# Kernel tuning notes

Hardware: AMD Instinct MI355X
Metric: run time of the kernel (lower is better)

Reference implementation:

```python
import jax, jax.numpy as jnp
import numpy as np

K_NEIGHBORS = 32  # n_neighbors, eval mode -> displacement = 0


def setup_inputs() -> dict:
    key = jax.random.key(0)
    ks = jax.random.split(key, 9)
    B, N, F = 1024, 200000, 64
    C, H = 16, 128
    return {
        "x": jax.random.normal(ks[0], (B, F), jnp.float32),
        "X_data": jax.random.normal(ks[1], (N, F), jnp.float32),
        "y": jax.random.uniform(ks[2], (N,), jnp.float32),
        "W_gate": jax.random.normal(ks[3], (F + 1, C), jnp.float32) / np.sqrt(F + 1),
        "b_gate": jax.random.normal(ks[4], (C,), jnp.float32) * 0.01,
        "W1": jax.random.normal(ks[5], (C + F, H), jnp.float32) / np.sqrt(C + F),
        "b1": jax.random.normal(ks[6], (H,), jnp.float32) * 0.01,
        "W_last": jax.random.normal(ks[7], (H, 1), jnp.float32) / np.sqrt(H),
        "b_last": jax.random.normal(ks[8], (1,), jnp.float32) * 0.01,
    }


def reference(x, X_data, y, W_gate, b_gate, W1, b1, W_last, b_last):
    # Euclidean (p=2) cdist via the expanded form: ||a-b||^2 = ||a||^2 + ||b||^2 - 2 a.b
    d2 = (jnp.sum(x * x, axis=1, keepdims=True)
          + jnp.sum(X_data * X_data, axis=1)[None, :]
          - 2.0 * (x @ X_data.T))                      # [B, N]
    dist = jnp.sqrt(jnp.maximum(d2, 0.0))
    # torch.argsort(distances,1)[:, :k] == indices of k smallest distances
    _, idx = jax.lax.top_k(-dist, K_NEIGHBORS)          # [B, K]
    neighbors = X_data[idx]                             # [B, K, F] gather
    neighbors_y = y[idx][..., None]                     # [B, K, 1]
    nf = jnp.concatenate([neighbors, neighbors_y], axis=2)  # [B, K, F+1]
    gated = jnp.tanh(nf @ W_gate + b_gate)              # [B, K, C]
    agg = jnp.sum(gated, axis=1)                        # [B, C]
    o = jnp.concatenate([x, agg], axis=1)               # [B, F+C]
    o = jnp.tanh(o @ W1 + b1)                           # activation_function = tanh
    o = jax.nn.sigmoid(o @ W_last + b_last)             # [B, 1]
    return o
```

## Files before the change

kernel.cpp:

```cpp
#include <hip/hip_runtime.h>
#include <cstdint>

#define FDIM 64
#define KNN 32
#define NBUCKET 256
#define MAXCAP 2048
#define SEG 10
#define OCAP 512

typedef unsigned int u32;
typedef unsigned long long u64;
typedef __attribute__((ext_vector_type(8))) short bf16x8;
typedef __attribute__((ext_vector_type(4))) float f32x4;

__device__ __forceinline__ float load_query(const float* __restrict__ x, int q, float4* xv) {
    const float4* xp = (const float4*)(x + (size_t)q * FDIM);
    float n0 = 0.f, n1 = 0.f, n2 = 0.f, n3 = 0.f;
#pragma unroll
    for (int k = 0; k < 16; ++k) {
        float4 v = xp[k];
        xv[k] = v;
        n0 = fmaf(v.x, v.x, n0); n1 = fmaf(v.y, v.y, n1);
        n2 = fmaf(v.z, v.z, n2); n3 = fmaf(v.w, v.w, n3);
    }
    return (n0 + n1) + (n2 + n3);
}

__device__ __forceinline__ float dot_row(const float4* __restrict__ xv, const float* __restrict__ row) {
    const float4* rv = (const float4*)row;
    float d0 = 0.f, d1 = 0.f, d2 = 0.f, d3 = 0.f;
#pragma unroll
    for (int k = 0; k < 16; ++k) {
        float4 r = rv[k];
        float4 a = xv[k];
        d0 = fmaf(a.x, r.x, d0); d1 = fmaf(a.y, r.y, d1);
        d2 = fmaf(a.z, r.z, d2); d3 = fmaf(a.w, r.w, d3);
    }
    return (d0 + d1) + (d2 + d3);
}

__global__ __launch_bounds__(256) void k_xnorm(const float* __restrict__ X, float* __restrict__ Xn, int N) {
    int i = blockIdx.x * 256 + threadIdx.x;
    if (i >= N) return;
    const float4* r = (const float4*)(X + (size_t)i * FDIM);
    float d0 = 0.f, d1 = 0.f, d2 = 0.f, d3 = 0.f;
#pragma unroll
    for (int k = 0; k < 16; ++k) {
        float4 v = r[k];
        d0 = fmaf(v.x, v.x, d0); d1 = fmaf(v.y, v.y, d1);
        d2 = fmaf(v.z, v.z, d2); d3 = fmaf(v.w, v.w, d3);
    }
    Xn[i] = (d0 + d1) + (d2 + d3);
}

__global__ __launch_bounds__(256) void k_cvtT(const float* __restrict__ src, uint4* __restrict__ dst, int n_u4) {
    int i = blockIdx.x * 256 + threadIdx.x;
    if (i >= n_u4) return;
    int lane = i & 63;
    int kk = (i >> 6) & 1;
    int g = i >> 7;
    int row = g * 16 + (lane & 15);
    int col = kk * 32 + (lane >> 4) * 8;
    const float4* s = (const float4*)(src + (size_t)row * FDIM + col);
    float4 a = s[0], b = s[1];
    ushort o[8];
    const float* f = &a.x;
#pragma unroll
    for (int k = 0; k < 4; ++k) {
        u32 u = __float_as_uint(f[k]);
        o[k] = (ushort)((u + 0x7fffu + ((u >> 16) & 1u)) >> 16);
    }
    const float* gg = &b.x;
#pragma unroll
    for (int k = 0; k < 4; ++k) {
        u32 u = __float_as_uint(gg[k]);
        o[4 + k] = (ushort)((u + 0x7fffu + ((u >> 16) & 1u)) >> 16);
    }
    dst[i] = *(uint4*)o;
}

__global__ __launch_bounds__(256) void k_hist(const float* __restrict__ x, const float* __restrict__ X,
                                              const float* __restrict__ Xn, u32* __restrict__ hist,
                                              int N, int nsamp, int sj) {
    __shared__ unsigned char h8[NBUCKET * 256];
    int t = threadIdx.x;
    u32* h32 = (u32*)h8;
#pragma unroll
    for (int k = 0; k < 64; ++k) h32[k * 256 + t] = 0;
    __syncthreads();
    int q = blockIdx.x * 256 + t;
    float4 xv[16];
    float xn = load_query(x, q, xv);
    for (int j = 0; j < sj; ++j) {
        int s = blockIdx.y * sj + j;
        int p = s * 16;
        if (s < nsamp && p < N) {
            float dp = dot_row(xv, X + (size_t)p * FDIM);
            float d2 = fmaxf(xn + Xn[p] - 2.f * dp, 0.f);
            int b = min(NBUCKET - 1, (int)d2);
            int idx = b * 256 + t;
            unsigned char v = h8[idx];
            h8[idx] = (v == 255u) ? v : (unsigned char)(v + 1);
        }
    }
    __syncthreads();
#pragma unroll
    for (int w = 0; w < 128; ++w) {
        u32 v0 = h8[(2 * w) * 256 + t];
        u32 v1 = h8[(2 * w + 1) * 256 + t];
        if (v0 | v1) atomicAdd(&hist[(size_t)q * 128 + w], v0 | (v1 << 16));
    }
}

__global__ __launch_bounds__(256) void k_thresh(const u32* __restrict__ hist, float* __restrict__ Tq, int B) {
    int q = blockIdx.x * 256 + threadIdx.x;
    if (q >= B) return;
    const u32* h = hist + (size_t)q * 128;
    int cum = 0;
    float T = (float)NBUCKET;
    for (int w = 0; w < 128; ++w) {
        u32 v = h[w];
        cum += (int)(v & 0xffffu);
        if (cum >= KNN) { T = (float)(2 * w + 1); break; }
        cum += (int)(v >> 16);
        if (cum >= KNN) { T = (float)(2 * w + 2); break; }
    }
    Tq[q] = T + 2.0f;
}

__global__ __launch_bounds__(256, 3) void k_sample_d2(
        const uint4* __restrict__ xT, const uint4* __restrict__ XT,
        const float* __restrict__ qn, const float* __restrict__ Xn,
        unsigned char* __restrict__ d2s, int S) {
    int t = threadIdx.x;
    int w = t >> 6, lane = t & 63;
    int G = lane >> 4, r = lane & 15;
    int qg = blockIdx.x;
    int wq = qg * 128 + w * 32;
    int pb = blockIdx.y * 128;

    bf16x8 afr[2][2];
#pragma unroll
    for (int kk = 0; kk < 2; ++kk)
#pragma unroll
        for (int mi = 0; mi < 2; ++mi) {
            uint4 v = xT[(size_t)(((wq >> 4) + mi) * 2 + kk) * 64 + lane];
            afr[kk][mi] = *(bf16x8*)&v;
        }
    float qr[8];
#pragma unroll
    for (int e = 0; e < 8; ++e)
        qr[e] = qn[wq + (e >> 2) * 16 + G * 4 + (e & 3)];

#pragma unroll
    for (int half = 0; half < 2; ++half) {
        int nb = half * 4;
        bf16x8 bfr[4][2];
#pragma unroll
        for (int j = 0; j < 4; ++j) {
            int gp = (pb >> 4) + nb + j;
#pragma unroll
            for (int kk = 0; kk < 2; ++kk) {
                uint4 v = XT[(size_t)(gp * 2 + kk) * 64 + lane];
                bfr[j][kk] = *(bf16x8*)&v;
            }
        }
        float xnv[4];
#pragma unroll
        for (int j = 0; j < 4; ++j) xnv[j] = Xn[pb + (nb + j) * 16 + r];

        f32x4 acc[2][4];
#pragma unroll
        for (int mi = 0; mi < 2; ++mi)
#pragma unroll
            for (int j = 0; j < 4; ++j) acc[mi][j] = (f32x4){0.f, 0.f, 0.f, 0.f};
#pragma unroll
        for (int kk = 0; kk < 2; ++kk)
#pragma unroll
            for (int j = 0; j < 4; ++j) {
                acc[0][j] = __builtin_amdgcn_mfma_f32_16x16x32_bf16(afr[kk][0], bfr[j][kk], acc[0][j], 0, 0, 0);
                acc[1][j] = __builtin_amdgcn_mfma_f32_16x16x32_bf16(afr[kk][1], bfr[j][kk], acc[1][j], 0, 0, 0);
            }
#pragma unroll
        for (int j = 0; j < 4; ++j) {
            int p = pb + (nb + j) * 16 + r;
            float xnp = xnv[j];
#pragma unroll
            for (int e = 0; e < 8; ++e) {
                float d2a = qr[e] + fmaf(-2.f, acc[e >> 2][j][e & 3], xnp);
                int b = (int)d2a;
                b = b < 0 ? 0 : (b > 255 ? 255 : b);
                int q = wq + (e >> 2) * 16 + G * 4 + (e & 3);
                d2s[(size_t)q * S + p] = (unsigned char)b;
            }
        }
    }
}

__global__ __launch_bounds__(256) void k_thresh2(const unsigned char* __restrict__ d2s,
                                                 float* __restrict__ Tq, int S) {
    __shared__ u32 h[NBUCKET];
    int t = threadIdx.x;
    int q = blockIdx.x;
    h[t] = 0;
    __syncthreads();
    const u32* row = (const u32*)(d2s + (size_t)q * S);
    int n4 = S >> 2;
    for (int i = t; i < n4; i += 256) {
        u32 v = row[i];
        atomicAdd(&h[v & 255u], 1u);
        atomicAdd(&h[(v >> 8) & 255u], 1u);
        atomicAdd(&h[(v >> 16) & 255u], 1u);
        atomicAdd(&h[v >> 24], 1u);
    }
    __syncthreads();
    if (t == 0) {
        int cum = 0;
        float T = 256.0f;
        for (int b = 0; b < NBUCKET; ++b) {
            cum += (int)h[b];
            if (cum >= KNN) { T = (float)(b + 1); break; }
        }
        Tq[q] = T + 2.0f;
    }
}

__global__ __launch_bounds__(256, 3) void k_mfma_filter(
        const uint4* __restrict__ xT, const uint4* __restrict__ XT,
        const float* __restrict__ qn, const float* __restrict__ Xn,
        const float* __restrict__ Tf,
        u32* __restrict__ cnt_seg, u32* __restrict__ list_seg,
        u32* __restrict__ ocnt, u32* __restrict__ olist,
        int N, int nStripsPad, int strip) {
    __shared__ u32 ldsCnt[128];

    int t = threadIdx.x;
    int w = t >> 6, lane = t & 63;
    int G = lane >> 4, r = lane & 15;

    int bid = blockIdx.x;
    int qg = (bid >> 3) & 7;
    int sIdx = (bid & 7) | ((bid >> 6) << 3);
    int qbase = qg * 128;
    int wq = qbase + w * 32;

    if (t < 128) ldsCnt[t] = 0;
    __syncthreads();

    bf16x8 afr[2][2];
#pragma unroll
    for (int kk = 0; kk < 2; ++kk)
#pragma unroll
        for (int mi = 0; mi < 2; ++mi) {
            uint4 v = xT[(size_t)(((wq >> 4) + mi) * 2 + kk) * 64 + lane];
            afr[kk][mi] = *(bf16x8*)&v;
        }
    float Tr[8];
#pragma unroll
    for (int e = 0; e < 8; ++e) {
        int rl = wq + (e >> 2) * 16 + G * 4 + (e & 3);
        Tr[e] = Tf[rl] - qn[rl];
    }

    u32* segBase = list_seg + ((size_t)qbase * nStripsPad + (size_t)sIdx) * SEG;

    for (int s = 0; s < strip; ++s) {
        int pb = (sIdx * strip + s) * 128;
        if (pb >= N) break;

#pragma unroll
        for (int half = 0; half < 2; ++half) {
            int nb = half * 4;
            bf16x8 bfr[4][2];
#pragma unroll
            for (int j = 0; j < 4; ++j) {
                int gp = (pb >> 4) + nb + j;
#pragma unroll
                for (int kk = 0; kk < 2; ++kk) {
                    uint4 v = XT[(size_t)(gp * 2 + kk) * 64 + lane];
                    bfr[j][kk] = *(bf16x8*)&v;
                }
            }
            float xnv[4];
#pragma unroll
            for (int j = 0; j < 4; ++j) xnv[j] = Xn[pb + (nb + j) * 16 + r];

            f32x4 acc[2][4];
#pragma unroll
            for (int mi = 0; mi < 2; ++mi)
#pragma unroll
                for (int j = 0; j < 4; ++j) acc[mi][j] = (f32x4){0.f, 0.f, 0.f, 0.f};
#pragma unroll
            for (int kk = 0; kk < 2; ++kk)
#pragma unroll
                for (int j = 0; j < 4; ++j) {
                    acc[0][j] = __builtin_amdgcn_mfma_f32_16x16x32_bf16(afr[kk][0], bfr[j][kk], acc[0][j], 0, 0, 0);
                    acc[1][j] = __builtin_amdgcn_mfma_f32_16x16x32_bf16(afr[kk][1], bfr[j][kk], acc[1][j], 0, 0, 0);
                }
#pragma unroll
            for (int j = 0; j < 4; ++j) {
                int p = pb + (nb + j) * 16 + r;
                float xnp = xnv[j];
                bool c0 = fmaf(-2.f, acc[0][j][0], xnp) < Tr[0];
                bool c1 = fmaf(-2.f, acc[0][j][1], xnp) < Tr[1];
                bool c2 = fmaf(-2.f, acc[0][j][2], xnp) < Tr[2];
                bool c3 = fmaf(-2.f, acc[0][j][3], xnp) < Tr[3];
                bool c4 = fmaf(-2.f, acc[1][j][0], xnp) < Tr[4];
                bool c5 = fmaf(-2.f, acc[1][j][1], xnp) < Tr[5];
                bool c6 = fmaf(-2.f, acc[1][j][2], xnp) < Tr[6];
                bool c7 = fmaf(-2.f, acc[1][j][3], xnp) < Tr[7];
                if ((c0 | c1 | c2 | c3 | c4 | c5 | c6 | c7) && p < N) {
#pragma unroll
                    for (int e = 0; e < 8; ++e) {
                        bool ce = (e == 0) ? c0 : (e == 1) ? c1 : (e == 2) ? c2 : (e == 3) ? c3
                                : (e == 4) ? c4 : (e == 5) ? c5 : (e == 6) ? c6 : c7;
                        if (ce) {
                            int ql = w * 32 + (e >> 2) * 16 + G * 4 + (e & 3);
                            u32 slot = atomicAdd(&ldsCnt[ql], 1u);
                            if (slot < SEG) {
                                segBase[(size_t)ql * nStripsPad * SEG + slot] = (u32)p;
                            } else {
                                u32 gs = atomicAdd(&ocnt[qbase + ql], 1u);
                                if (gs < OCAP) olist[(size_t)(qbase + ql) * OCAP + gs] = (u32)p;
                            }
                        }
                    }
                }
            }
        }
    }

    __syncthreads();
    if (t < 128) cnt_seg[(size_t)(qbase + t) * nStripsPad + sIdx] = min(ldsCnt[t], (u32)SEG);
}

__global__ __launch_bounds__(256) void k_filter_scalar(const float* __restrict__ x, const float* __restrict__ X,
                                                       const float* __restrict__ Xn, const float* __restrict__ Tq,
                                                       u32* __restrict__ cnt, u32* __restrict__ list,
                                                       int N, int cap) {
    int t = threadIdx.x;
    int q = blockIdx.x * 256 + t;
    float4 xv[16];
    float xn = load_query(x, q, xv);
    float T = Tq[q];
    int base = blockIdx.y * 1024;
    int lim = min(1024, N - base);
    for (int j = 0; j < lim; ++j) {
        int p = base + j;
        float dp = dot_row(xv, X + (size_t)p * FDIM);
        float d2 = fmaxf(xn + Xn[p] - 2.f * dp, 0.f);
        if (d2 < T) {
            u32 slot = atomicAdd(&cnt[q], 1u);
            if (slot < (u32)cap) list[(size_t)q * cap + slot] = (u32)p;
        }
    }
}

__global__ __launch_bounds__(256) void k_final(const float* __restrict__ x, const float* __restrict__ X,
                                               const float* __restrict__ y, const float* __restrict__ Xn,
                                               const float* __restrict__ Wg, const float* __restrict__ bg,
                                               const float* __restrict__ W1, const float* __restrict__ b1,
                                               const float* __restrict__ Wl, const float* __restrict__ bl,
                                               const u32* __restrict__ cnt_seg, const u32* __restrict__ list_seg,
                                               const u32* __restrict__ ocnt, const u32* __restrict__ olist,
                                               const u32* __restrict__ cnt_flat, const u32* __restrict__ list_flat,
                                               float* __restrict__ out, int nStripsPad, int cap_flat, int flat,
                                               int N) {
    __shared__ u64 keys[MAXCAP];
    __shared__ u32 nsh;
    __shared__ u64 wk[4];
    __shared__ int wp[4];
    __shared__ u32 sel[KNN];
    __shared__ float gkc[KNN * 16];
    __shared__ float aggc[16];
    __shared__ float red[128];

    int t = threadIdx.x;
    int w = t >> 6, lane = t & 63;
    int q = blockIdx.x;
    int m;

    if (flat) {
        m = (int)min(cnt_flat[q], (u32)cap_flat);
        const u32* lq = list_flat + (size_t)q * cap_flat;
        for (int i = t; i < m; i += 256) keys[i] = lq[i];
    } else {
        if (t == 0) nsh = 0;
        __syncthreads();
        for (int seg = t; seg < nStripsPad; seg += 256) {
            u32 c = cnt_seg[(size_t)q * nStripsPad + seg];
            if (c) {
                u32 base = atomicAdd(&nsh, c);
                const u32* sp = list_seg + ((size_t)q * nStripsPad + seg) * SEG;
                for (u32 j = 0; j < c; ++j) {
                    u32 idx = base + j;
                    if (idx < MAXCAP) keys[idx] = sp[j];
                }
            }
        }
        __syncthreads();
        int m0 = (int)min(nsh, (u32)MAXCAP);
        int oc = (int)min(ocnt[q], (u32)OCAP);
        for (int i = t; i < oc; i += 256)
            if (m0 + i < MAXCAP) keys[m0 + i] = olist[(size_t)q * OCAP + i];
        m = min(m0 + oc, MAXCAP);
    }
    __syncthreads();

    {
        int ch = lane & 15;
        int rsub = lane >> 4;
        float4 xq4 = ((const float4*)(x + (size_t)q * FDIM))[ch];
        float xs = fmaf(xq4.x, xq4.x, fmaf(xq4.y, xq4.y, fmaf(xq4.z, xq4.z, xq4.w * xq4.w)));
        xs += __shfl_xor(xs, 1);
        xs += __shfl_xor(xs, 2);
        xs += __shfl_xor(xs, 4);
        xs += __shfl_xor(xs, 8);
        float xn = xs;
        for (int base = w * 32; base < m; base += 128) {
            int ri[8]; u32 pp[8]; bool val[8]; float4 vv[8];
#pragma unroll
            for (int u = 0; u < 8; ++u) {
                ri[u] = base + u * 4 + rsub;
                val[u] = ri[u] < m;
                pp[u] = val[u] ? (u32)keys[ri[u]] : 0u;
            }
#pragma unroll
            for (int u = 0; u < 8; ++u)
                vv[u] = ((const float4*)(X + (size_t)pp[u] * FDIM))[ch];
#pragma unroll
            for (int u = 0; u < 8; ++u) {
                float part = fmaf(xq4.x, vv[u].x, fmaf(xq4.y, vv[u].y, fmaf(xq4.z, vv[u].z, xq4.w * vv[u].w)));
                part += __shfl_xor(part, 1);
                part += __shfl_xor(part, 2);
                part += __shfl_xor(part, 4);
                part += __shfl_xor(part, 8);
                if (val[u] && ch == 0) {
                    float d2 = fmaxf(xn + Xn[pp[u]] - 2.f * part, 0.f);
                    keys[ri[u]] = ((u64)__float_as_uint(d2) << 32) | pp[u];
                }
            }
        }
    }
    __syncthreads();

    if (m <= 512) {
        if (w == 0) {
            u64 rk[8];
#pragma unroll
            for (int i = 0; i < 8; ++i) {
                int idx = lane + (i << 6);
                rk[i] = (idx < m) ? keys[idx] : ~0ull;
            }
            for (int r = 0; r < KNN; ++r) {
                u64 bk = ~0ull;
                int bs = 0;
#pragma unroll
                for (int i = 0; i < 8; ++i)
                    if (rk[i] < bk) { bk = rk[i]; bs = i; }
                int bo = lane;
#pragma unroll
                for (int off = 1; off < 64; off <<= 1) {
                    u64 ok = __shfl_xor(bk, off);
                    int oo = __shfl_xor(bo, off);
                    if (ok < bk) { bk = ok; bo = oo; }
                }
                if (lane == bo) rk[bs] = ~0ull;
                if (lane == 0) sel[r] = (u32)bk;
            }
        }
        __syncthreads();
    } else {
        for (int r = 0; r < KNN; ++r) {
            u64 bk = ~0ull;
            int bp = -1;
            for (int i = t; i < m; i += 256) {
                u64 k = keys[i];
                if (k < bk) { bk = k; bp = i; }
            }
#pragma unroll
            for (int off = 32; off > 0; off >>= 1) {
                u64 ok = __shfl_down(bk, off);
                int op = __shfl_down(bp, off);
                if (ok < bk) { bk = ok; bp = op; }
            }
            if (lane == 0) { wk[w] = bk; wp[w] = bp; }
            __syncthreads();
            if (t == 0) {
                u64 fb = wk[0];
                int fp = wp[0];
                for (int v = 1; v < 4; ++v)
                    if (wk[v] < fb) { fb = wk[v]; fp = wp[v]; }
                sel[r] = (u32)(fb & 0xffffffffu);
                if (fp >= 0) keys[fp] = ~0ull;
            }
            __syncthreads();
        }
    }

    int c = t & 15, kk = t >> 4;
#pragma unroll
    for (int rep = 0; rep < 2; ++rep) {
        int k = kk + 16 * rep;
        int nb = min((int)sel[k], N - 1);
        const float* Xr = X + (size_t)nb * FDIM;
        float acc = bg[c];
#pragma unroll
        for (int f = 0; f < FDIM; ++f) acc = fmaf(Xr[f], Wg[f * 16 + c], acc);
        acc = fmaf(y[nb], Wg[FDIM * 16 + c], acc);
        gkc[k * 16 + c] = tanhf(acc);
    }
    __syncthreads();
    if (t < 16) {
        float s = 0.f;
#pragma unroll
        for (int k = 0; k < KNN; ++k) s += gkc[k * 16 + t];
        aggc[t] = s;
    }
    __syncthreads();
    if (t < 128) {
        const float* xq = x + (size_t)q * FDIM;
        float acc = b1[t];
#pragma unroll
        for (int f = 0; f < FDIM; ++f) acc = fmaf(xq[f], W1[f * 128 + t], acc);
#pragma unroll
        for (int cc2 = 0; cc2 < 16; ++cc2) acc = fmaf(aggc[cc2], W1[(FDIM + cc2) * 128 + t], acc);
        red[t] = tanhf(acc) * Wl[t];
    }
    __syncthreads();
    for (int off = 64; off > 0; off >>= 1) {
        if (t < off) red[t] += red[t + off];
        __syncthreads();
    }
    if (t == 0) out[q] = 1.f / (1.f + expf(-(red[0] + bl[0])));
}

extern "C" void kernel_launch(void* const* d_in, const int* in_sizes, int n_in,
                              void* d_out, int out_size, void* d_ws, size_t ws_size,
                              hipStream_t stream) {
    const float* x  = (const float*)d_in[0];
    const float* X  = (const float*)d_in[1];
    const float* y  = (const float*)d_in[2];
    const float* Wg = (const float*)d_in[3];
    const float* bg = (const float*)d_in[4];
    const float* W1 = (const float*)d_in[5];
    const float* b1 = (const float*)d_in[6];
    const float* Wl = (const float*)d_in[7];
    const float* bl = (const float*)d_in[8];
    float* out = (float*)d_out;

    int B = in_sizes[0] / FDIM;
    int N = in_sizes[1] / FDIM;

    const int strip = 8;
    int nTiles = (N + 127) / 128;
    int nStrips = (nTiles + strip - 1) / strip;
    nStrips = (nStrips + 7) & ~7;
    int nStripsPad = nStrips;
    int Npad = nStrips * strip * 128;

    char* w = (char*)d_ws;
    size_t off = 0;
    auto alloc = [&](size_t bytes) { void* p = w + off; off += (bytes + 255) & ~(size_t)255; return p; };
    float* Xn  = (float*)alloc((size_t)Npad * 4);
    float* qn  = (float*)alloc((size_t)B * 4);
    u32* hist  = (u32*)alloc((size_t)B * 512);
    float* Tq  = (float*)alloc((size_t)B * 4);
    u32* cnt   = (u32*)alloc((size_t)B * 4);

    size_t xTB = (size_t)B * 128;
    size_t XTB = (size_t)(Npad / 16) * 2048;
    size_t segCntB = (size_t)B * nStripsPad * 4;
    size_t segListB = (size_t)B * nStripsPad * SEG * 4;
    size_t ocntB = (size_t)B * 4;
    size_t olistB = (size_t)B * OCAP * 4;
    size_t rem = (ws_size > off) ? ws_size - off : 0;
    bool mfma_path = rem >= xTB + XTB + segCntB + segListB + ocntB + olistB + 4096;

    uint4* xT = nullptr; uint4* XT = nullptr;
    u32 *cnt_seg = nullptr, *list_seg = nullptr, *ocnt = nullptr, *olist = nullptr;
    u32* list_flat = nullptr; unsigned char* d2s = nullptr;
    int cap_flat = 64, Stiles = 0;
    if (mfma_path) {
        xT = (uint4*)alloc(xTB);
        XT = (uint4*)alloc(XTB);
        cnt_seg  = (u32*)alloc(segCntB);
        list_seg = (u32*)alloc(segListB);
        ocnt     = (u32*)alloc(ocntB);
        olist    = (u32*)alloc(olistB);
        rem = (ws_size > off) ? ws_size - off : 0;
        size_t st = rem / ((size_t)B * 128);
        Stiles = st > 198 ? 198 : (int)st;
        int maxFull = N / 128;
        if (Stiles > maxFull) Stiles = maxFull;
        if (Stiles >= 96) d2s = (unsigned char*)alloc((size_t)Stiles * 128 * B);
        else Stiles = 0;
    } else {
        size_t c = rem / ((size_t)B * 4);
        cap_flat = c > MAXCAP ? MAXCAP : (int)c;
        if (cap_flat < 64) cap_flat = 64;
        list_flat = (u32*)alloc((size_t)B * cap_flat * 4);
    }

    k_xnorm<<<dim3((N + 255) / 256), 256, 0, stream>>>(X, Xn, N);
    k_xnorm<<<dim3((B + 255) / 256), 256, 0, stream>>>(x, qn, B);

    if (mfma_path) {
        hipMemsetAsync(ocnt, 0, ocntB, stream);
        hipMemsetAsync(Xn + N, 0, (size_t)(Npad - N) * 4, stream);
        size_t realXT = (size_t)(N / 16) * 2048;
        hipMemsetAsync((char*)XT + realXT, 0, XTB - realXT, stream);

        int nxu4 = B * 8, nXu4 = N * 8;
        k_cvtT<<<dim3((nxu4 + 255) / 256), 256, 0, stream>>>(x, xT, nxu4);
        k_cvtT<<<dim3((nXu4 + 255) / 256), 256, 0, stream>>>(X, XT, nXu4);

        if (Stiles > 0) {
            int S = Stiles * 128;
            k_sample_d2<<<dim3(8, Stiles), 256, 0, stream>>>(xT, XT, qn, Xn, d2s, S);
            k_thresh2<<<dim3(B), 256, 0, stream>>>(d2s, Tq, S);
        } else {
            hipMemsetAsync(hist, 0, (size_t)B * 512, stream);
            int nsamp = (N + 15) / 16;
            int chunks = 128;
            int sj = (nsamp + chunks - 1) / chunks;
            k_hist<<<dim3(B / 256, chunks), 256, 0, stream>>>(x, X, Xn, hist, N, nsamp, sj);
            k_thresh<<<dim3((B + 255) / 256), 256, 0, stream>>>(hist, Tq, B);
        }

        k_mfma_filter<<<dim3(8 * nStrips), 256, 0, stream>>>(
            xT, XT, qn, Xn, Tq, cnt_seg, list_seg, ocnt, olist, N, nStripsPad, strip);

        k_final<<<dim3(B), 256, 0, stream>>>(x, X, y, Xn, Wg, bg, W1, b1, Wl, bl,
                                             cnt_seg, list_seg, ocnt, olist,
                                             nullptr, nullptr, out, nStripsPad, 0, 0, N);
    } else {
        hipMemsetAsync(cnt, 0, (size_t)B * 4, stream);
        hipMemsetAsync(hist, 0, (size_t)B * 512, stream);
        int nsamp = (N + 15) / 16;
        int chunks = 128;
        int sj = (nsamp + chunks - 1) / chunks;
        k_hist<<<dim3(B / 256, chunks), 256, 0, stream>>>(x, X, Xn, hist, N, nsamp, sj);
        k_thresh<<<dim3((B + 255) / 256), 256, 0, stream>>>(hist, Tq, B);
        k_filter_scalar<<<dim3(B / 256, (N + 1023) / 1024), 256, 0, stream>>>(
            x, X, Xn, Tq, cnt, list_flat, N, cap_flat);
        k_final<<<dim3(B), 256, 0, stream>>>(x, X, y, Xn, Wg, bg, W1, b1, Wl, bl,
                                             nullptr, nullptr, nullptr, nullptr,
                                             cnt, list_flat, out, nStripsPad, cap_flat, 1, N);
    }
}
```

Before: 288.2 us.

## Pack quantized approximate distance into candidate keys and prefilter before exact rescoring

The filter kernel now stores a 14-bit quantized approximate squared distance alongside the 18-bit point index in each candidate key. The final kernel builds a histogram over these coarse distances, finds the bucket holding the 32nd nearest, and keeps only candidates within a margin band above it. Only those go through the exact fp32 distance recompute and top-k selection, cutting X gathers and selection work. This adds a histogram pass and scan, limits indices to 2^18 points, and relies on the bf16 error margin (BANDQ) being wide enough not to drop true neighbors.

```diff
diff --git a/kernel.cpp b/kernel.cpp
--- a/kernel.cpp
+++ b/kernel.cpp
@@ -7,6 +7,7 @@
 #define MAXCAP 2048
 #define SEG 10
 #define OCAP 512
+#define BANDQ 96
 
 typedef unsigned int u32;
 typedef unsigned long long u64;
@@ -255,11 +256,13 @@
             uint4 v = xT[(size_t)(((wq >> 4) + mi) * 2 + kk) * 64 + lane];
             afr[kk][mi] = *(bf16x8*)&v;
         }
-    float Tr[8];
+    float Tr[8], qnr[8];
 #pragma unroll
     for (int e = 0; e < 8; ++e) {
         int rl = wq + (e >> 2) * 16 + G * 4 + (e & 3);
-        Tr[e] = Tf[rl] - qn[rl];
+        float qv = qn[rl];
+        qnr[e] = qv;
+        Tr[e] = Tf[rl] - qv;
     }
 
     u32* segBase = list_seg + ((size_t)qbase * nStripsPad + (size_t)sIdx) * SEG;
@@ -301,27 +304,29 @@
             for (int j = 0; j < 4; ++j) {
                 int p = pb + (nb + j) * 16 + r;
                 float xnp = xnv[j];
-                bool c0 = fmaf(-2.f, acc[0][j][0], xnp) < Tr[0];
-                bool c1 = fmaf(-2.f, acc[0][j][1], xnp) < Tr[1];
-                bool c2 = fmaf(-2.f, acc[0][j][2], xnp) < Tr[2];
-                bool c3 = fmaf(-2.f, acc[0][j][3], xnp) < Tr[3];
-                bool c4 = fmaf(-2.f, acc[1][j][0], xnp) < Tr[4];
-                bool c5 = fmaf(-2.f, acc[1][j][1], xnp) < Tr[5];
-                bool c6 = fmaf(-2.f, acc[1][j][2], xnp) < Tr[6];
-                bool c7 = fmaf(-2.f, acc[1][j][3], xnp) < Tr[7];
-                if ((c0 | c1 | c2 | c3 | c4 | c5 | c6 | c7) && p < N) {
+                float dv[8];
+                bool ce[8];
+#pragma unroll
+                for (int e = 0; e < 8; ++e) {
+                    dv[e] = fmaf(-2.f, acc[e >> 2][j][e & 3], xnp);
+                    ce[e] = dv[e] < Tr[e];
+                }
+                if ((ce[0] | ce[1] | ce[2] | ce[3] | ce[4] | ce[5] | ce[6] | ce[7]) && p < N) {
 #pragma unroll
                     for (int e = 0; e < 8; ++e) {
-                        bool ce = (e == 0) ? c0 : (e == 1) ? c1 : (e == 2) ? c2 : (e == 3) ? c3
-                                : (e == 4) ? c4 : (e == 5) ? c5 : (e == 6) ? c6 : c7;
-                        if (ce) {
+                        if (ce[e]) {
+                            float d2a = dv[e] + qnr[e];
+                            d2a = d2a < 0.f ? 0.f : d2a;
+                            u32 dq = (u32)(d2a * 32.f);
+                            if (dq > 16383u) dq = 16383u;
+                            u32 key = (dq << 18) | (u32)p;
                             int ql = w * 32 + (e >> 2) * 16 + G * 4 + (e & 3);
                             u32 slot = atomicAdd(&ldsCnt[ql], 1u);
                             if (slot < SEG) {
-                                segBase[(size_t)ql * nStripsPad * SEG + slot] = (u32)p;
+                                segBase[(size_t)ql * nStripsPad * SEG + slot] = key;
                             } else {
                                 u32 gs = atomicAdd(&ocnt[qbase + ql], 1u);
-                                if (gs < OCAP) olist[(size_t)(qbase + ql) * OCAP + gs] = (u32)p;
+                                if (gs < OCAP) olist[(size_t)(qbase + ql) * OCAP + gs] = key;
                             }
                         }
                     }
@@ -374,6 +379,10 @@
     __shared__ float gkc[KNN * 16];
     __shared__ float aggc[16];
     __shared__ float red[128];
+    __shared__ u32 hist[2048];
+    __shared__ u32 wtot[4];
+    __shared__ u32 cutq_sh;
+    __shared__ u32 nrs;
 
     int t = threadIdx.x;
     int w = t >> 6, lane = t & 63;
@@ -407,6 +416,49 @@
     }
     __syncthreads();
 
+    if (!flat) {
+        for (int i = t; i < 2048; i += 256) hist[i] = 0;
+        if (t == 0) cutq_sh = 0xFFFFFFFFu;
+        __syncthreads();
+        for (int i = t; i < m; i += 256) atomicAdd(&hist[((u32)keys[i]) >> 21], 1u);
+        __syncthreads();
+        u32 s = 0;
+#pragma unroll
+        for (int j = 0; j < 8; ++j) s += hist[t * 8 + j];
+        u32 run = s;
+#pragma unroll
+        for (int off = 1; off < 64; off <<= 1) {
+            u32 v = __shfl_up(run, off);
+            if (lane >= off) run += v;
+        }
+        if (lane == 63) wtot[w] = run;
+        __syncthreads();
+        u32 wo = 0;
+#pragma unroll
+        for (int v = 0; v < 4; ++v) wo += (v < w) ? wtot[v] : 0u;
+        u32 inc = wo + run;
+        u32 exc = inc - s;
+        if (exc < (u32)KNN && inc >= (u32)KNN) {
+            u32 cum = exc;
+#pragma unroll
+            for (int j = 0; j < 8; ++j) {
+                cum += hist[t * 8 + j];
+                if (cum >= (u32)KNN) { cutq_sh = (u32)(((t * 8 + j + 1) << 3) + BANDQ); break; }
+            }
+        }
+    }
+    if (t == 0) nrs = 0;
+    __syncthreads();
+    u32 cutq = flat ? 0xFFFFFFFFu : cutq_sh;
+
+    u32* cand = hist;
+    for (int i = t; i < m; i += 256) {
+        u32 k = (u32)keys[i];
+        if ((k >> 18) <= cutq) cand[atomicAdd(&nrs, 1u)] = k & 0x3FFFFu;
+    }
+    __syncthreads();
+    int mr = (int)min(nrs, (u32)MAXCAP);
+
     {
         int ch = lane & 15;
         int rsub = lane >> 4;
@@ -417,13 +469,13 @@
         xs += __shfl_xor(xs, 4);
         xs += __shfl_xor(xs, 8);
         float xn = xs;
-        for (int base = w * 32; base < m; base += 128) {
+        for (int base = w * 32; base < mr; base += 128) {
             int ri[8]; u32 pp[8]; bool val[8]; float4 vv[8];
 #pragma unroll
             for (int u = 0; u < 8; ++u) {
                 ri[u] = base + u * 4 + rsub;
-                val[u] = ri[u] < m;
-                pp[u] = val[u] ? (u32)keys[ri[u]] : 0u;
+                val[u] = ri[u] < mr;
+                pp[u] = val[u] ? cand[ri[u]] : 0u;
             }
 #pragma unroll
             for (int u = 0; u < 8; ++u)
@@ -444,13 +496,13 @@
     }
     __syncthreads();
 
-    if (m <= 512) {
+    if (mr <= 512) {
         if (w == 0) {
             u64 rk[8];
 #pragma unroll
             for (int i = 0; i < 8; ++i) {
                 int idx = lane + (i << 6);
-                rk[i] = (idx < m) ? keys[idx] : ~0ull;
+                rk[i] = (idx < mr) ? keys[idx] : ~0ull;
             }
             for (int r = 0; r < KNN; ++r) {
                 u64 bk = ~0ull;
@@ -474,7 +526,7 @@
         for (int r = 0; r < KNN; ++r) {
             u64 bk = ~0ull;
             int bp = -1;
-            for (int i = t; i < m; i += 256) {
+            for (int i = t; i < mr; i += 256) {
                 u64 k = keys[i];
                 if (k < bk) { bk = k; bp = i; }
             }
```

Result: faster. 261.8 us (-9.2%).
